# Kernel optimization log

Hardware: AMD Instinct MI355X
Metric: run time of the kernel (lower is better)

Reference implementation:

```python
import jax, jax.numpy as jnp
import numpy as np

N_NODES = 4194304  # 2**22
LEVELS = 10
COARSE = 8192
RANK = 2
NNZ = 8388608


def _interp_linear(u, N):
    """torch F.interpolate(mode='linear', align_corners=False) along axis 1. u: (B,M,R) -> (B,N,R)."""
    M = u.shape[1]
    pos = (jnp.arange(N, dtype=jnp.float32) + 0.5) * (M / N) - 0.5
    pos = jnp.clip(pos, 0.0, M - 1)
    i0 = jnp.floor(pos).astype(jnp.int32)
    i1 = jnp.minimum(i0 + 1, M - 1)
    w = (pos - i0.astype(jnp.float32))[None, :, None]
    return u[:, i0] * (1.0 - w) + u[:, i1] * w


def _apply_hodlr(diag, u_factors, v_factors, x):
    B, N, _ = x.shape
    y = diag * x
    L = u_factors.shape[0]
    for lvl in range(L):
        num_splits = 2 ** (lvl + 1)
        bs = N // num_splits
        if bs == 0:
            continue
        uc, vc = u_factors[lvl], v_factors[lvl]
        u_full = _interp_linear(uc, N) if uc.shape[1] != N else uc
        v_full = _interp_linear(vc, N) if vc.shape[1] != N else vc
        P = num_splits // 2
        valid = P * 2 * bs
        xv = x[:, :valid].reshape(B, P, 2, bs, 1)
        uv = u_full[:, :valid].reshape(B, P, 2, bs, -1)
        vv = v_full[:, :valid].reshape(B, P, 2, bs, -1)
        xL, xR = xv[:, :, 0], xv[:, :, 1]
        uL, uR = uv[:, :, 0], uv[:, :, 1]
        vL, vR = vv[:, :, 0], vv[:, :, 1]
        xRp = jnp.einsum('bpkr,bpko->bpro', vR, xR)  # (B,P,R,1)
        xLp = jnp.einsum('bpkr,bpko->bpro', vL, xL)
        yL = jnp.einsum('bpkr,bpro->bpko', uL, xRp)  # (B,P,bs,1)
        yR = jnp.einsum('bpkr,bpro->bpko', uR, xLp)
        upd = jnp.stack([yL, yR], axis=2).reshape(B, valid, 1)
        if valid < N:
            upd = jnp.pad(upd, ((0, 0), (0, N - valid), (0, 0)))
        y = y + upd
    return y


def setup_inputs() -> dict:
    key = jax.random.key(0)
    ks = jax.random.split(key, 6)
    diag = jax.random.uniform(ks[0], (1, N_NODES, 1), dtype=jnp.float32)
    u_factors = jax.random.normal(ks[1], (LEVELS, 1, COARSE, RANK), dtype=jnp.float32)
    v_factors = jax.random.normal(ks[2], (LEVELS, 1, COARSE, RANK), dtype=jnp.float32)
    A_values = jax.random.normal(ks[3], (NNZ,), dtype=jnp.float32)
    z = jax.random.normal(ks[4], (1, N_NODES, 1), dtype=jnp.float32)
    A_indices = jax.random.randint(ks[5], (2, NNZ), 0, N_NODES, dtype=jnp.int64) if jax.config.jax_enable_x64 else jax.random.randint(ks[5], (2, NNZ), 0, N_NODES, dtype=jnp.int32)
    return {"diag": diag, "u_factors": u_factors, "v_factors": v_factors,
            "A_values": A_values, "z": z, "A_indices": A_indices, "num_nodes": N_NODES}


def reference(diag, u_factors, v_factors, A_values, z, A_indices, num_nodes):
    N = num_nodes
    w = _apply_hodlr(diag, u_factors, v_factors, z)          # (1,N,1)
    w_flat = w.reshape(N)
    rows, cols = A_indices[0], A_indices[1]
    y_flat = jax.ops.segment_sum(A_values * w_flat[cols], rows, num_segments=N)
    y = y_flat.reshape(1, N, 1)
    loss = jnp.mean((y - z) ** 2)
    return loss
```

## Files before the change

### kernel.cpp

```cpp
#include <hip/hip_runtime.h>

#define N_NODES 4194304
#define LEVELS  10
#define COARSE  8192
#define NNZ_E   8388608
#define NSEG    512
#define RB_SZ   8192
#define EPB     8192
#define CAP_SEG 18432u

typedef int          v4i __attribute__((ext_vector_type(4)));
typedef float        v4f __attribute__((ext_vector_type(4)));
typedef unsigned int v4u __attribute__((ext_vector_type(4)));

static __device__ __forceinline__ unsigned short f2bf(float x) {
    unsigned u = __float_as_uint(x);
    return (unsigned short)((u + 0x7FFFu + ((u >> 16) & 1u)) >> 16);
}
static __device__ __forceinline__ float bf2f(unsigned short h) {
    return __uint_as_float((unsigned)h << 16);
}

__global__ __launch_bounds__(512) void k1(const float* __restrict__ z,
                                          float2* __restrict__ M,
                                          float* __restrict__ S,
                                          float* __restrict__ out) {
    int b = blockIdx.x, t = threadIdx.x;
    if (b == 0) {
        for (int i = t; i < 2046 * 2; i += 512) S[i] = 0.f;
        if (t == 0) out[0] = 0.f;
    }
    int lane = t & 63, wave = t >> 6;
    int chunk = b * 8 + wave;
    int base = chunk * 256 + lane * 4;
    float4 zv = *(const float4*)(z + base);
    float a0 = 0.f, a1 = 0.f;
    const float* zp = (const float*)&zv;
#pragma unroll
    for (int j = 0; j < 4; ++j) {
        float p = ((float)(base + j) + 0.5f) * (1.0f / 512.0f) - 0.5f;
        p = fminf(fmaxf(p, 0.0f), (float)(COARSE - 1));
        float f = p - floorf(p);
        a0 += zp[j] * (1.0f - f);
        a1 += zp[j] * f;
    }
#pragma unroll
    for (int off = 32; off >= 1; off >>= 1) {
        a0 += __shfl_xor(a0, off, 64);
        a1 += __shfl_xor(a1, off, 64);
    }
    if (lane == 0) M[chunk] = make_float2(a0, a1);
}

__global__ __launch_bounds__(256) void kB(const float2* __restrict__ M,
                                          const float* __restrict__ V,
                                          float* __restrict__ S) {
    int b = blockIdx.x, t = threadIdx.x;
    int lvl = b >> 3, slice = b & 7;
    const float2* Vl = (const float2*)(V + lvl * COARSE * 2);
    float s0 = 0.f, s1 = 0.f;
    int c0 = slice * 2048 + t * 8;
#pragma unroll
    for (int cc = 0; cc < 8; ++cc) {
        int c = c0 + cc;
        float2 m = M[c];
        int k = (c > 0) ? ((c - 1) >> 1) : 0;
        int kp = min(k + 1, COARSE - 1);
        float2 vk = Vl[k], vkp = Vl[kp];
        s0 += vk.x * m.x + vkp.x * m.y;
        s1 += vk.y * m.x + vkp.y * m.y;
    }
    int gw = min(1 << (10 - lvl), 64);
    for (int sh = gw >> 1; sh >= 1; sh >>= 1) {
        s0 += __shfl_xor(s0, sh, 64);
        s1 += __shfl_xor(s1, sh, 64);
    }
    if ((t & (gw - 1)) == 0) {
        int bb = c0 >> (13 - lvl);
        int soff = (2 << lvl) - 2;
        unsafeAtomicAdd(&S[(soff + bb) * 2 + 0], s0);
        unsafeAtomicAdd(&S[(soff + bb) * 2 + 1], s1);
    }
}

__global__ __launch_bounds__(512) void kCw(const float* __restrict__ diag,
                                           const float* __restrict__ z,
                                           const float* __restrict__ S,
                                           const float* __restrict__ U,
                                           unsigned short* __restrict__ wb) {
    int b = blockIdx.x, t = threadIdx.x;
    int tid = b * 512 + t;
    int base = tid * 4;
    int c = base >> 8;
    int k = (c > 0) ? ((c - 1) >> 1) : 0;
    int kp = min(k + 1, COARSE - 1);
    float g0 = 0.f, g1 = 0.f;
#pragma unroll
    for (int lvl = 0; lvl < LEVELS; ++lvl) {
        int sib = (c >> (13 - lvl)) ^ 1;
        int soff = (2 << lvl) - 2;
        float2 s2 = ((const float2*)S)[soff + sib];
        const float2* Ul = (const float2*)(U + lvl * COARSE * 2);
        float2 uk = Ul[k], ukp = Ul[kp];
        g0 += uk.x * s2.x + uk.y * s2.y;
        g1 += ukp.x * s2.x + ukp.y * s2.y;
    }
    float4 d4 = *(const float4*)(diag + base);
    float4 z4 = *(const float4*)(z + base);
    const float* dp = (const float*)&d4;
    const float* zp = (const float*)&z4;
    ushort4 h4;
    unsigned short* hp = (unsigned short*)&h4;
#pragma unroll
    for (int j = 0; j < 4; ++j) {
        float p = ((float)(base + j) + 0.5f) * (1.0f / 512.0f) - 0.5f;
        p = fminf(fmaxf(p, 0.0f), (float)(COARSE - 1));
        float f = p - floorf(p);
        hp[j] = f2bf(dp[j] * zp[j] + (g0 + f * (g1 - g0)));
    }
    *(ushort4*)(wb + base) = h4;
}

__global__ __launch_bounds__(1024) void k2(const int* __restrict__ rows,
                                           const int* __restrict__ cols,
                                           const float* __restrict__ vals,
                                           const unsigned short* __restrict__ wb,
                                           unsigned* __restrict__ segCtr,
                                           unsigned* __restrict__ binned) {
    __shared__ unsigned sortedP[EPB];
    __shared__ unsigned short sortedB[EPB];
    __shared__ unsigned cur[NSEG], gb[NSEG];
    __shared__ unsigned wsum[16], wbase[16];
    int blk = blockIdx.x, t = threadIdx.x;
    int base = blk * EPB;
    v4i r[2], c[2];
    v4f v[2];
#pragma unroll
    for (int j = 0; j < 2; ++j) {
        int e = base + j * 4096 + t * 4;
        r[j] = __builtin_nontemporal_load((const v4i*)(rows + e));
        c[j] = __builtin_nontemporal_load((const v4i*)(cols + e));
        v[j] = __builtin_nontemporal_load((const v4f*)(vals + e));
    }
    float wf[8];
#pragma unroll
    for (int j = 0; j < 2; ++j) {
        const int* cp = (const int*)&c[j];
#pragma unroll
        for (int kk = 0; kk < 4; ++kk)
            wf[j * 4 + kk] = bf2f(wb[(unsigned)cp[kk]]);
    }
    if (t < NSEG) cur[t] = 0u;
    __syncthreads();
#pragma unroll
    for (int j = 0; j < 2; ++j) {
        const int* rp = (const int*)&r[j];
#pragma unroll
        for (int kk = 0; kk < 4; ++kk)
            atomicAdd(&cur[(unsigned)rp[kk] >> 13], 1u);
    }
    __syncthreads();
    unsigned lv = 0, lincl = 0;
    if (t < NSEG) {
        lv = cur[t];
        lincl = lv;
#pragma unroll
        for (int off = 1; off < 64; off <<= 1) {
            unsigned n = __shfl_up(lincl, off, 64);
            if ((t & 63) >= off) lincl += n;
        }
        if ((t & 63) == 63) wsum[t >> 6] = lincl;
    }
    __syncthreads();
    if (t == 0) {
        unsigned a = 0;
        for (int i = 0; i < 8; ++i) { wbase[i] = a; a += wsum[i]; }
    }
    __syncthreads();
    if (t < NSEG) {
        unsigned lexcl = wbase[t >> 6] + lincl - lv;
        gb[t] = (unsigned)t * CAP_SEG + atomicAdd(&segCtr[t], lv) - lexcl;
        cur[t] = lexcl;
    }
    __syncthreads();
#pragma unroll
    for (int j = 0; j < 2; ++j) {
        const int* rp = (const int*)&r[j];
        const float* vp = (const float*)&v[j];
#pragma unroll
        for (int kk = 0; kk < 4; ++kk) {
            unsigned row = (unsigned)rp[kk];
            unsigned seg = row >> 13;
            unsigned rl = row & 8191u;
            float p = wf[j * 4 + kk] * vp[kk];
            unsigned pe = ((__float_as_uint(p) + 0x1000u) >> 13) & 0x7FFFFu;
            unsigned i = atomicAdd(&cur[seg], 1u);
            sortedP[i] = (rl << 19) | pe;
            sortedB[i] = (unsigned short)seg;
        }
    }
    __syncthreads();
#pragma unroll
    for (int k = 0; k < 8; ++k) {
        int i = k * 1024 + t;
        unsigned s = sortedB[i];
        __builtin_nontemporal_store(sortedP[i], binned + gb[s] + i);
    }
}

__global__ __launch_bounds__(1024) void kE(const unsigned* __restrict__ binned,
                                           const unsigned* __restrict__ segCtr,
                                           const float* __restrict__ z,
                                           float* __restrict__ out) {
    __shared__ float acc[RB_SZ];
    __shared__ float red[16];
    int b = blockIdx.x, t = threadIdx.x;

    for (int i = t; i < RB_SZ / 4; i += 1024) ((float4*)acc)[i] = make_float4(0.f, 0.f, 0.f, 0.f);
    __syncthreads();

    unsigned n = segCtr[b];
    const unsigned* seg = binned + (size_t)b * CAP_SEG;
    unsigned i = t;
    for (; i + 7u * 1024u < n; i += 8u * 1024u) {
        unsigned ev[8];
#pragma unroll
        for (int k = 0; k < 8; ++k)
            ev[k] = __builtin_nontemporal_load(seg + i + (unsigned)k * 1024u);
#pragma unroll
        for (int k = 0; k < 8; ++k)
            atomicAdd(&acc[ev[k] >> 19], __uint_as_float((ev[k] & 0x7FFFFu) << 13));
    }
    for (; i < n; i += 1024u) {
        unsigned e = __builtin_nontemporal_load(seg + i);
        atomicAdd(&acc[e >> 19], __uint_as_float((e & 0x7FFFFu) << 13));
    }
    __syncthreads();

    float part = 0.f;
    int gbase = b * RB_SZ;
    for (int k = t; k < RB_SZ; k += 1024) {
        float d = acc[k] - z[gbase + k];
        part += d * d;
    }
#pragma unroll
    for (int off = 32; off >= 1; off >>= 1) part += __shfl_xor(part, off, 64);
    if ((t & 63) == 0) red[t >> 6] = part;
    __syncthreads();
    if (t == 0) {
        float s = 0.f;
        for (int k = 0; k < 16; ++k) s += red[k];
        unsafeAtomicAdd(out, s * (1.0f / (float)N_NODES));
    }
}

extern "C" void kernel_launch(void* const* d_in, const int* in_sizes, int n_in,
                              void* d_out, int out_size, void* d_ws, size_t ws_size,
                              hipStream_t stream) {
    const float* diag  = (const float*)d_in[0];
    const float* U     = (const float*)d_in[1];
    const float* V     = (const float*)d_in[2];
    const float* Avals = (const float*)d_in[3];
    const float* z     = (const float*)d_in[4];
    const int*   Aidx  = (const int*)d_in[5];
    const int* rows = Aidx;
    const int* cols = Aidx + NNZ_E;

    char* ws = (char*)d_ws;
    size_t off = 0;
    unsigned short* wb  = (unsigned short*)(ws + off); off += (size_t)N_NODES * 2;
    unsigned* binned    = (unsigned*)(ws + off);       off += (size_t)NSEG * CAP_SEG * 4;
    unsigned* segCtr    = (unsigned*)(ws + off);       off += NSEG * 4;
    float2* M           = (float2*)(ws + off);         off += (size_t)(N_NODES / 256) * 8;
    float* S            = (float*)(ws + off);          off += 16384;

    hipMemsetAsync(segCtr, 0, NSEG * 4, stream);
    k1<<<2048, 512, 0, stream>>>(z, M, S, (float*)d_out);
    kB<<<80, 256, 0, stream>>>(M, V, S);
    kCw<<<2048, 512, 0, stream>>>(diag, z, S, U, wb);
    k2<<<1024, 1024, 0, stream>>>(rows, cols, Avals, wb, segCtr, binned);
    kE<<<NSEG, 1024, 0, stream>>>(binned, segCtr, z, (float*)d_out);
}
```

Measured before the change: 317.8 us.

## Replace row-binned scatter with direct global float atomics on y

Drops the two-pass scheme that binned packed (row, reduced-precision product) entries into per-segment buffers and then reduced them in LDS. Each edge now atomically adds its product straight into a full-size float y array in global memory. Columns are handled in four passes by column range, with a block barrier between passes, to improve locality of the bf16 w gathers. A separate kernel then computes the squared-error loss. This removes the binned-buffer write and read-back and the LDS sorting work. In exchange it adds a 16 MB memset of y and 8M scattered global atomics, which may contend or be slow in L2.

Result: slower. 595.1 us (+87.2%).

```diff
diff --git a/kernel.cpp b/kernel.cpp
--- a/kernel.cpp
+++ b/kernel.cpp
@@ -4,14 +4,9 @@
 #define LEVELS  10
 #define COARSE  8192
 #define NNZ_E   8388608
-#define NSEG    512
-#define RB_SZ   8192
-#define EPB     8192
-#define CAP_SEG 18432u
 
 typedef int          v4i __attribute__((ext_vector_type(4)));
 typedef float        v4f __attribute__((ext_vector_type(4)));
-typedef unsigned int v4u __attribute__((ext_vector_type(4)));
 
 static __device__ __forceinline__ unsigned short f2bf(float x) {
     unsigned u = __float_as_uint(x);
@@ -121,135 +116,59 @@
     *(ushort4*)(wb + base) = h4;
 }
 
-__global__ __launch_bounds__(1024) void k2(const int* __restrict__ rows,
-                                           const int* __restrict__ cols,
-                                           const float* __restrict__ vals,
-                                           const unsigned short* __restrict__ wb,
-                                           unsigned* __restrict__ segCtr,
-                                           unsigned* __restrict__ binned) {
-    __shared__ unsigned sortedP[EPB];
-    __shared__ unsigned short sortedB[EPB];
-    __shared__ unsigned cur[NSEG], gb[NSEG];
-    __shared__ unsigned wsum[16], wbase[16];
+__global__ __launch_bounds__(512) void k2(const int* __restrict__ rows,
+                                          const int* __restrict__ cols,
+                                          const float* __restrict__ vals,
+                                          const unsigned short* __restrict__ wb,
+                                          float* __restrict__ y) {
     int blk = blockIdx.x, t = threadIdx.x;
-    int base = blk * EPB;
+    int base = blk * 4096;
     v4i r[2], c[2];
     v4f v[2];
 #pragma unroll
     for (int j = 0; j < 2; ++j) {
-        int e = base + j * 4096 + t * 4;
+        int e = base + j * 2048 + t * 4;
         r[j] = __builtin_nontemporal_load((const v4i*)(rows + e));
         c[j] = __builtin_nontemporal_load((const v4i*)(cols + e));
         v[j] = __builtin_nontemporal_load((const v4f*)(vals + e));
     }
-    float wf[8];
-#pragma unroll
-    for (int j = 0; j < 2; ++j) {
-        const int* cp = (const int*)&c[j];
-#pragma unroll
-        for (int kk = 0; kk < 4; ++kk)
-            wf[j * 4 + kk] = bf2f(wb[(unsigned)cp[kk]]);
-    }
-    if (t < NSEG) cur[t] = 0u;
-    __syncthreads();
-#pragma unroll
-    for (int j = 0; j < 2; ++j) {
-        const int* rp = (const int*)&r[j];
-#pragma unroll
-        for (int kk = 0; kk < 4; ++kk)
-            atomicAdd(&cur[(unsigned)rp[kk] >> 13], 1u);
-    }
-    __syncthreads();
-    unsigned lv = 0, lincl = 0;
-    if (t < NSEG) {
-        lv = cur[t];
-        lincl = lv;
-#pragma unroll
-        for (int off = 1; off < 64; off <<= 1) {
-            unsigned n = __shfl_up(lincl, off, 64);
-            if ((t & 63) >= off) lincl += n;
+#pragma unroll 1
+    for (int p = 0; p < 4; ++p) {
+#pragma unroll
+        for (int j = 0; j < 2; ++j) {
+            const int* rp = (const int*)&r[j];
+            const int* cp = (const int*)&c[j];
+            const float* vp = (const float*)&v[j];
+#pragma unroll
+            for (int kk = 0; kk < 4; ++kk) {
+                unsigned cc = (unsigned)cp[kk];
+                if ((cc >> 20) == (unsigned)p) {
+                    float w = bf2f(wb[cc]);
+                    unsafeAtomicAdd(&y[(unsigned)rp[kk]], vp[kk] * w);
+                }
+            }
         }
-        if ((t & 63) == 63) wsum[t >> 6] = lincl;
-    }
-    __syncthreads();
-    if (t == 0) {
-        unsigned a = 0;
-        for (int i = 0; i < 8; ++i) { wbase[i] = a; a += wsum[i]; }
-    }
-    __syncthreads();
-    if (t < NSEG) {
-        unsigned lexcl = wbase[t >> 6] + lincl - lv;
-        gb[t] = (unsigned)t * CAP_SEG + atomicAdd(&segCtr[t], lv) - lexcl;
-        cur[t] = lexcl;
-    }
-    __syncthreads();
-#pragma unroll
-    for (int j = 0; j < 2; ++j) {
-        const int* rp = (const int*)&r[j];
-        const float* vp = (const float*)&v[j];
-#pragma unroll
-        for (int kk = 0; kk < 4; ++kk) {
-            unsigned row = (unsigned)rp[kk];
-            unsigned seg = row >> 13;
-            unsigned rl = row & 8191u;
-            float p = wf[j * 4 + kk] * vp[kk];
-            unsigned pe = ((__float_as_uint(p) + 0x1000u) >> 13) & 0x7FFFFu;
-            unsigned i = atomicAdd(&cur[seg], 1u);
-            sortedP[i] = (rl << 19) | pe;
-            sortedB[i] = (unsigned short)seg;
-        }
-    }
-    __syncthreads();
-#pragma unroll
-    for (int k = 0; k < 8; ++k) {
-        int i = k * 1024 + t;
-        unsigned s = sortedB[i];
-        __builtin_nontemporal_store(sortedP[i], binned + gb[s] + i);
-    }
-}
-
-__global__ __launch_bounds__(1024) void kE(const unsigned* __restrict__ binned,
-                                           const unsigned* __restrict__ segCtr,
-                                           const float* __restrict__ z,
-                                           float* __restrict__ out) {
-    __shared__ float acc[RB_SZ];
-    __shared__ float red[16];
-    int b = blockIdx.x, t = threadIdx.x;
-
-    for (int i = t; i < RB_SZ / 4; i += 1024) ((float4*)acc)[i] = make_float4(0.f, 0.f, 0.f, 0.f);
-    __syncthreads();
-
-    unsigned n = segCtr[b];
-    const unsigned* seg = binned + (size_t)b * CAP_SEG;
-    unsigned i = t;
-    for (; i + 7u * 1024u < n; i += 8u * 1024u) {
-        unsigned ev[8];
-#pragma unroll
-        for (int k = 0; k < 8; ++k)
-            ev[k] = __builtin_nontemporal_load(seg + i + (unsigned)k * 1024u);
-#pragma unroll
-        for (int k = 0; k < 8; ++k)
-            atomicAdd(&acc[ev[k] >> 19], __uint_as_float((ev[k] & 0x7FFFFu) << 13));
-    }
-    for (; i < n; i += 1024u) {
-        unsigned e = __builtin_nontemporal_load(seg + i);
-        atomicAdd(&acc[e >> 19], __uint_as_float((e & 0x7FFFFu) << 13));
-    }
-    __syncthreads();
-
-    float part = 0.f;
-    int gbase = b * RB_SZ;
-    for (int k = t; k < RB_SZ; k += 1024) {
-        float d = acc[k] - z[gbase + k];
-        part += d * d;
-    }
+        __syncthreads();
+    }
+}
+
+__global__ __launch_bounds__(512) void kL(const float* __restrict__ y,
+                                          const float* __restrict__ z,
+                                          float* __restrict__ out) {
+    __shared__ float red[8];
+    int b = blockIdx.x, t = threadIdx.x;
+    int base = (b * 512 + t) * 4;
+    float4 y4 = *(const float4*)(y + base);
+    float4 z4 = *(const float4*)(z + base);
+    float d0 = y4.x - z4.x, d1 = y4.y - z4.y, d2 = y4.z - z4.z, d3 = y4.w - z4.w;
+    float part = d0 * d0 + d1 * d1 + d2 * d2 + d3 * d3;
 #pragma unroll
     for (int off = 32; off >= 1; off >>= 1) part += __shfl_xor(part, off, 64);
     if ((t & 63) == 0) red[t >> 6] = part;
     __syncthreads();
     if (t == 0) {
         float s = 0.f;
-        for (int k = 0; k < 16; ++k) s += red[k];
+        for (int i = 0; i < 8; ++i) s += red[i];
         unsafeAtomicAdd(out, s * (1.0f / (float)N_NODES));
     }
 }
@@ -269,15 +188,14 @@
     char* ws = (char*)d_ws;
     size_t off = 0;
     unsigned short* wb  = (unsigned short*)(ws + off); off += (size_t)N_NODES * 2;
-    unsigned* binned    = (unsigned*)(ws + off);       off += (size_t)NSEG * CAP_SEG * 4;
-    unsigned* segCtr    = (unsigned*)(ws + off);       off += NSEG * 4;
+    float* y            = (float*)(ws + off);          off += (size_t)N_NODES * 4;
     float2* M           = (float2*)(ws + off);         off += (size_t)(N_NODES / 256) * 8;
     float* S            = (float*)(ws + off);          off += 16384;
 
-    hipMemsetAsync(segCtr, 0, NSEG * 4, stream);
+    hipMemsetAsync(y, 0, (size_t)N_NODES * 4, stream);
     k1<<<2048, 512, 0, stream>>>(z, M, S, (float*)d_out);
     kB<<<80, 256, 0, stream>>>(M, V, S);
     kCw<<<2048, 512, 0, stream>>>(diag, z, S, U, wb);
-    k2<<<1024, 1024, 0, stream>>>(rows, cols, Avals, wb, segCtr, binned);
-    kE<<<NSEG, 1024, 0, stream>>>(binned, segCtr, z, (float*)d_out);
-}
+    k2<<<2048, 512, 0, stream>>>(rows, cols, Avals, wb, y);
+    kL<<<2048, 512, 0, stream>>>(y, z, (float*)d_out);
+}
```
